# Optimization experiments

Hardware: AMD Instinct MI355X
Metric: run time of the kernel (lower is better)

The kernel has to match this reference:

```python
import jax, jax.numpy as jnp
import numpy as np

L = 50
N_INIT = 3.5      # initial radius n
N_STEP = 0.5      # n_step
NUM_ADJ_PARM = 0.1
NUM_CANDS = 256   # candidate radii n + k*n_step


def _leaky(x):
    return jax.nn.leaky_relu(x, negative_slope=0.01)


def _conv(x, w, b):
    y = jax.lax.conv_general_dilated(x, w, (1, 1), 'VALID',
                                     dimension_numbers=('NCHW', 'OIHW', 'NCHW'))
    return y + b[None, :, None, None]


def _maxpool2(x):
    return jax.lax.reduce_window(x, -jnp.inf, jax.lax.max,
                                 (1, 1, 2, 2), (1, 1, 2, 2), 'VALID')


def _sage(x, adj, w_rel, b_rel, w_root):
    # PyG DenseSAGEConv: lin_rel(mean-agg) + lin_root(x), normalize=False
    agg = adj @ x
    deg = jnp.clip(jnp.sum(adj, axis=-1, keepdims=True), 1.0, None)
    return (agg / deg) @ w_rel.T + b_rel + x @ w_root.T


def _build_adj(h):
    # fused pairwise euclidean distance + radius threshold with retry:
    # smallest radius in {n + k*n_step} whose (directed) edge count >= 0.1*N
    g = h @ h.T                                   # [N,N] gram
    sq = jnp.diag(g)
    dist = jnp.sqrt(jnp.maximum(sq[:, None] - 2.0 * g + sq[None, :], 0.0))
    n = h.shape[0]
    eye = jnp.eye(n, dtype=bool)
    d_sorted = jnp.sort(jnp.where(eye, jnp.inf, dist).reshape(-1))
    cands = N_INIT + N_STEP * jnp.arange(NUM_CANDS, dtype=dist.dtype)
    counts = jnp.searchsorted(d_sorted, cands)    # edges with dist < cand
    thr = cands[jnp.argmax(counts >= NUM_ADJ_PARM * n)]
    A = ((dist < thr) & (~eye)).astype(h.dtype)
    return jax.lax.stop_gradient(A)               # edge list is non-diff in torch too


def _diff_pool(z, a, s):
    # PyG dense_diff_pool (link + entropy losses; only link loss l1 is returned)
    s = jax.nn.softmax(s, axis=-1)
    x = s.T @ z
    adj = s.T @ a @ s
    l1 = jnp.linalg.norm(a - s @ s.T) / (a.shape[0] * a.shape[1])
    return x, adj, l1


def setup_inputs() -> dict:
    key = jax.random.key(0)
    ks = jax.random.split(key, 19)
    def w(k, shape, scale=0.05):
        return scale * jax.random.normal(k, shape, dtype=jnp.float32)
    N = 4096  # bag size / number of graph nodes
    return {
        'x': jax.random.normal(ks[0], (1, N, 1, 28, 28), dtype=jnp.float32),
        'conv1_w': w(ks[1], (20, 1, 5, 5)),
        'conv1_b': w(ks[2], (20,)),
        'conv2_w': w(ks[3], (50, 20, 5, 5)),
        'conv2_b': w(ks[4], (50,)),
        'fc_w': w(ks[5], (50, 800)),
        'fc_b': w(ks[6], (50,)),
        'embd_rel_w': w(ks[7], (50, 50)),
        'embd_rel_b': w(ks[8], (50,)),
        'embd_root_w': w(ks[9], (50, 50)),
        'pool_rel_w': w(ks[10], (1, 50)),
        'pool_rel_b': w(ks[11], (1,)),
        'pool_root_w': w(ks[12], (1, 50)),
        'mlp_w': w(ks[13], (1, 1)),
        'mlp_b': w(ks[14], (1,)),
        'lin1_w': w(ks[15], (25, 50)),
        'lin1_b': w(ks[16], (25,)),
        'lin2_w': w(ks[17], (2, 25)),
        'lin2_b': w(ks[18], (2,)),
    }


def reference(x, conv1_w, conv1_b, conv2_w, conv2_b, fc_w, fc_b,
              embd_rel_w, embd_rel_b, embd_root_w,
              pool_rel_w, pool_rel_b, pool_root_w,
              mlp_w, mlp_b, lin1_w, lin1_b, lin2_w, lin2_b):
    xi = x[0]                                             # squeeze(0): [N,1,28,28]
    h = _maxpool2(jax.nn.relu(_conv(xi, conv1_w, conv1_b)))   # [N,20,12,12]
    h = _maxpool2(jax.nn.relu(_conv(h, conv2_w, conv2_b)))    # [N,50,4,4]
    h = h.reshape(h.shape[0], -1)                         # [N,800]
    h = jax.nn.relu(h @ fc_w.T + fc_b)                    # [N,50]
    A = _build_adj(h)                                     # [N,N] dense adjacency
    Z = _leaky(_sage(h, A, embd_rel_w, embd_rel_b, embd_root_w))   # [N,50]
    S = _leaky(_sage(h, A, pool_rel_w, pool_rel_b, pool_root_w))   # [N,1]
    S = _leaky(S @ mlp_w.T + mlp_b)                       # [N,1]
    Xp, adjp, l1 = _diff_pool(Z, A, S)                    # [1,50], [1,1]
    Xp = _leaky(_sage(Xp, adjp, embd_rel_w, embd_rel_b, embd_root_w))  # reuses gnn_embd
    v = Xp.reshape(-1)                                    # [50]
    v = _leaky(v @ lin1_w.T + lin1_b)                     # [25]
    v = _leaky(v @ lin2_w.T + lin2_b)                     # [2]
    p = jax.nn.softmax(v, axis=0)
    return jnp.max(p), jnp.argmax(p), l1
```

## Files before the change

### kernel.cpp

```cpp
#include <hip/hip_runtime.h>
#include <hip/hip_bf16.h>

#define AGG_OFF     0u
#define DEG_OFF     819200u
#define XP_OFF      835584u
#define HIST_OFF    835840u
#define SCAL_OFF    836992u
#define S_OFF       837120u
#define H_OFF       1048576u
#define HT_OFF      1867776u
#define SQ_OFF      2686976u
#define BYTES_OFF   2703360u
#define WS_NEED     (2703360ull + 16777216ull)

__global__ __launch_bounds__(256) void mil_init(unsigned int* __restrict__ w)
{
    w[(size_t)blockIdx.x * 256u + threadIdx.x] = 0u;
}

__global__ __launch_bounds__(256) void mil_cnn(
    const float* __restrict__ x, const float* __restrict__ w1, const float* __restrict__ b1,
    const float* __restrict__ w2, const float* __restrict__ b2,
    const float* __restrict__ fcw, const float* __restrict__ fcb,
    float* __restrict__ hout, float* __restrict__ hT, float* __restrict__ sqout)
{
    __shared__ __align__(16) float img[784];
    __shared__ float w1s[500];
    __shared__ float b1s[20];
    __shared__ float b2s[50];
    __shared__ __align__(16) float pool1[20*144];
    __shared__ float w2s[50*4*25];
    __shared__ __align__(16) float pool2[800];
    __shared__ float hloc[50];

    const int n = blockIdx.x;
    const int t = threadIdx.x;

    const float* xin = x + (size_t)n * 784;
    for (int i = t; i < 784; i += 256) img[i] = xin[i];
    for (int i = t; i < 500; i += 256) w1s[i] = w1[i];
    if (t < 20) b1s[t] = b1[t];
    { int u = t - 32; if (u >= 0 && u < 50) b2s[u] = b2[u]; }
    __syncthreads();

    if (t < 240) {
        const int c = t / 12, py = t % 12;
        float wr[25];
#pragma unroll
        for (int k = 0; k < 25; k++) wr[k] = w1s[c*25 + k];
        float acc0[24], acc1[24];
#pragma unroll
        for (int i = 0; i < 24; i++) { acc0[i] = 0.f; acc1[i] = 0.f; }
#pragma unroll
        for (int ky = 0; ky < 5; ky++) {
            const int yr = 2*py + ky;
            float ra[28], rb[28];
#pragma unroll
            for (int i = 0; i < 28; i++) ra[i] = img[yr*28 + i];
#pragma unroll
            for (int i = 0; i < 28; i++) rb[i] = img[yr*28 + 28 + i];
#pragma unroll
            for (int kx = 0; kx < 5; kx++) {
                const float wv = wr[ky*5 + kx];
#pragma unroll
                for (int xo = 0; xo < 24; xo++) {
                    acc0[xo] = fmaf(ra[xo+kx], wv, acc0[xo]);
                    acc1[xo] = fmaf(rb[xo+kx], wv, acc1[xo]);
                }
            }
        }
        const float bias = b1s[c];
#pragma unroll
        for (int px = 0; px < 12; px++) {
            float v = fmaxf(fmaxf(acc0[2*px], acc0[2*px+1]),
                            fmaxf(acc1[2*px], acc1[2*px+1]));
            pool1[c*144 + py*12 + px] = fmaxf(v + bias, 0.f);
        }
    }
    __syncthreads();

    float acc2[16];
#pragma unroll
    for (int i = 0; i < 16; i++) acc2[i] = 0.f;
    const int c2 = t / 4, py2 = t % 4;
    for (int cig = 0; cig < 5; cig++) {
        __syncthreads();
        for (int idx = t; idx < 5000; idx += 256) {
            const int cc = idx / 100, rem = idx % 100;
            w2s[idx] = w2[cc*500 + cig*100 + rem];
        }
        __syncthreads();
        if (t < 200) {
#pragma unroll
            for (int cl = 0; cl < 4; cl++) {
                const int cig4 = cig*4 + cl;
#pragma unroll
                for (int ky = 0; ky < 5; ky++) {
                    const int r = 2*py2 + ky;
                    float ra[12], rb[12];
#pragma unroll
                    for (int i = 0; i < 12; i++) ra[i] = pool1[cig4*144 + r*12 + i];
#pragma unroll
                    for (int i = 0; i < 12; i++) rb[i] = pool1[cig4*144 + (r+1)*12 + i];
#pragma unroll
                    for (int kx = 0; kx < 5; kx++) {
                        const float wv = w2s[(c2*4 + cl)*25 + ky*5 + kx];
#pragma unroll
                        for (int xo = 0; xo < 8; xo++) {
                            acc2[xo]   = fmaf(ra[xo+kx], wv, acc2[xo]);
                            acc2[8+xo] = fmaf(rb[xo+kx], wv, acc2[8+xo]);
                        }
                    }
                }
            }
        }
    }
    __syncthreads();
    if (t < 200) {
        const float bias = b2s[c2];
#pragma unroll
        for (int px = 0; px < 4; px++) {
            float v = fmaxf(fmaxf(acc2[2*px], acc2[2*px+1]),
                            fmaxf(acc2[8+2*px], acc2[8+2*px+1]));
            pool2[c2*16 + py2*4 + px] = fmaxf(v + bias, 0.f);
        }
    }
    __syncthreads();

    {
        const int wv = t >> 6, lane = t & 63;
        for (int o = wv; o < 50; o += 4) {
            float acc = 0.f;
#pragma unroll
            for (int r = 0; r < 13; r++) {
                const int k = r*64 + lane;
                if (k < 800) acc = fmaf(fcw[o*800 + k], pool2[k], acc);
            }
#pragma unroll
            for (int off = 32; off > 0; off >>= 1) acc += __shfl_xor(acc, off);
            if (lane == 0) hloc[o] = fmaxf(acc + fcb[o], 0.f);
        }
    }
    __syncthreads();
    if (t < 50) {
        const float v = hloc[t];
        hout[(size_t)n*50 + t] = v;
        hT[(size_t)t*4096 + n] = v;
    }
    if (t < 64) {
        float s = (t < 50) ? hloc[t]*hloc[t] : 0.f;
#pragma unroll
        for (int off = 32; off > 0; off >>= 1) s += __shfl_xor(s, off);
        if (t == 0) sqout[n] = s;
    }
}

__global__ __launch_bounds__(256) void mil_colsum(
    const float* __restrict__ hT, float* __restrict__ S)
{
    __shared__ float red[4];
    const int d = blockIdx.x, t = threadIdx.x;
    float s = 0.f;
    for (int nn = t; nn < 4096; nn += 256) s += hT[(size_t)d*4096 + nn];
#pragma unroll
    for (int off = 32; off > 0; off >>= 1) s += __shfl_xor(s, off);
    if ((t & 63) == 0) red[t >> 6] = s;
    __syncthreads();
    if (t == 0) S[d] = red[0] + red[1] + red[2] + red[3];
}

__global__ __launch_bounds__(256, 3) void mil_hist(
    const float* __restrict__ hT, const float* __restrict__ sq,
    unsigned int* __restrict__ hist, unsigned char* __restrict__ bytesA,
    const int wb)
{
    __shared__ __align__(16) float hiT[6400];
    __shared__ __align__(16) float hjT[6400];
    __shared__ float sqi[128], sqj[128];
    __shared__ unsigned int lh[257];

    const int t = threadIdx.x;
    const int i0 = blockIdx.x * 128, j0 = blockIdx.y * 128;

    for (int idx = t; idx < 6400; idx += 256) {
        const int c = idx >> 7, l = idx & 127;
        hiT[idx] = hT[(size_t)c*4096 + i0 + l];
        hjT[idx] = hT[(size_t)c*4096 + j0 + l];
    }
    if (t < 128) { sqi[t] = sq[i0 + t]; sqj[t] = sq[j0 + t]; }
    for (int idx = t; idx < 257; idx += 256) lh[idx] = 0;
    __syncthreads();

    const int ti = t >> 4, tj = t & 15;
    float acc[8][8];
#pragma unroll
    for (int a = 0; a < 8; a++)
#pragma unroll
        for (int b = 0; b < 8; b++) acc[a][b] = 0.f;

    for (int c = 0; c < 50; c++) {
        const float4 a0 = *(const float4*)&hiT[c*128 + ti*8];
        const float4 a1 = *(const float4*)&hiT[c*128 + ti*8 + 4];
        const float4 b0 = *(const float4*)&hjT[c*128 + tj*8];
        const float4 b1 = *(const float4*)&hjT[c*128 + tj*8 + 4];
        const float aa[8] = {a0.x,a0.y,a0.z,a0.w,a1.x,a1.y,a1.z,a1.w};
        const float bb[8] = {b0.x,b0.y,b0.z,b0.w,b1.x,b1.y,b1.z,b1.w};
#pragma unroll
        for (int a = 0; a < 8; a++)
#pragma unroll
            for (int b = 0; b < 8; b++)
                acc[a][b] = fmaf(aa[a], bb[b], acc[a][b]);
    }

    unsigned int cnt0 = 0;
#pragma unroll
    for (int a = 0; a < 8; a++) {
        unsigned pk0 = 0, pk1 = 0;
#pragma unroll
        for (int b = 0; b < 8; b++) {
            const int gi = i0 + ti*8 + a, gj = j0 + tj*8 + b;
            int kbyte = 255;
            if (gi != gj) {
                const float d2 = sqi[ti*8+a] + sqj[tj*8+b] - 2.f*acc[a][b];
                const float d = sqrtf(fmaxf(d2, 0.f));
                int k = (int)floorf((d - 3.5f)*2.f) + 1;
                k = k < 0 ? 0 : (k > 256 ? 256 : k);
                if (k > 0   && d <  3.5f + 0.5f*(float)(k-1)) k--;
                if (k < 256 && d >= 3.5f + 0.5f*(float)k)     k++;
                if (k == 0) cnt0++;
                else atomicAdd(&lh[k], 1u);
                kbyte = k < 255 ? k : 255;
            }
            if (b < 4) pk0 |= (unsigned)kbyte << (8*b);
            else       pk1 |= (unsigned)kbyte << (8*(b-4));
        }
        if (wb) {
            const int gi = i0 + ti*8 + a;
            *(uint2*)&bytesA[(size_t)gi*4096 + j0 + tj*8] = make_uint2(pk0, pk1);
        }
    }
#pragma unroll
    for (int off = 32; off > 0; off >>= 1) cnt0 += __shfl_xor(cnt0, off);
    if ((t & 63) == 0 && cnt0) atomicAdd(&lh[0], cnt0);
    __syncthreads();
    for (int idx = t; idx < 257; idx += 256)
        if (lh[idx]) atomicAdd(&hist[idx], lh[idx]);
}

__global__ void mil_scan(const unsigned int* __restrict__ hist, int* __restrict__ scal)
{
    if (threadIdx.x == 0) {
        unsigned long long cum = 0, nz = 0;
        int kc = -1;
        for (int k = 0; k < 256; k++) {
            cum += hist[k];
            if (kc < 0 && cum >= 410ull) { kc = k; nz = cum; }
        }
        if (kc < 0) { kc = 0; nz = hist[0]; }
        scal[0] = kc;
        scal[1] = (int)nz;
        scal[2] = (nz * 2ull > 16773120ull) ? 1 : 0;
        scal[3] = (kc >= 255) ? 1 : 0;
    }
}

__global__ __launch_bounds__(256) void mil_agg_b(
    const float* __restrict__ h, const unsigned char* __restrict__ bytesA,
    const int* __restrict__ scal, float* __restrict__ agg, float* __restrict__ deg)
{
    __shared__ __align__(16) unsigned char bL[64*528];
    __shared__ __align__(16) float hsub[4096];
    if (scal[3] != 0) return;
    const int t = threadIdx.x;
    const int i0 = blockIdx.x * 64;
    const int jg = blockIdx.y * 512;
    const int kc = scal[0];
    const bool inv = (scal[2] != 0);

    for (int idx = t; idx < 2048; idx += 256) {
        const int r = idx >> 5, c = idx & 31;
        *(uint4*)&bL[r*528 + c*16] =
            *(const uint4*)&bytesA[(size_t)(i0 + r)*4096 + jg + c*16];
    }

    const int il = t >> 2, dq = t & 3;
    const int gi = i0 + il;
    float accum[16];
#pragma unroll
    for (int i = 0; i < 16; i++) accum[i] = 0.f;
    int degc = 0;

    for (int js = 0; js < 8; js++) {
        __syncthreads();
        for (int idx = t; idx < 4096; idx += 256) {
            const int jj = idx >> 6, d = idx & 63;
            hsub[idx] = (d < 50) ? h[(size_t)(jg + js*64 + jj)*50 + d] : 0.f;
        }
        __syncthreads();
        const unsigned char* brow = &bL[il*528 + js*64];
        const int jbase = jg + js*64;
        for (int jj = 0; jj < 64; jj++) {
            const bool e = (jbase + jj != gi) && ((brow[jj] <= kc) != inv);
            if (!__any(e)) continue;
            const float m = e ? 1.f : 0.f;
            if (e && dq == 0) degc++;
#pragma unroll
            for (int q = 0; q < 4; q++) {
                const float4 hv = *(const float4*)&hsub[jj*64 + dq*16 + q*4];
                accum[q*4+0] = fmaf(m, hv.x, accum[q*4+0]);
                accum[q*4+1] = fmaf(m, hv.y, accum[q*4+1]);
                accum[q*4+2] = fmaf(m, hv.z, accum[q*4+2]);
                accum[q*4+3] = fmaf(m, hv.w, accum[q*4+3]);
            }
        }
    }

#pragma unroll
    for (int q = 0; q < 4; q++)
#pragma unroll
        for (int rr = 0; rr < 4; rr++) {
            const int d = dq*16 + q*4 + rr;
            if (d < 50 && accum[q*4+rr] != 0.f)
                atomicAdd(&agg[(size_t)gi*50 + d], accum[q*4+rr]);
        }
    if (dq == 0 && degc) atomicAdd(&deg[gi], (float)degc);
}

__global__ __launch_bounds__(256, 3) void mil_agg_r(
    const float* __restrict__ h, const float* __restrict__ hT, const float* __restrict__ sq,
    const int* __restrict__ scal, float* __restrict__ agg, float* __restrict__ deg,
    const int mode)
{
    __shared__ __align__(16) float hiT[3200];
    __shared__ __align__(16) float hjT[3200];
    __shared__ float sqi[64], sqj[64];
    __shared__ __align__(16) float hsub[4096];
    __shared__ __align__(16) unsigned char mk[4096];

    if (mode == 1 && scal[3] == 0) return;
    const int t = threadIdx.x;
    const int i0 = blockIdx.x * 64;
    const float thr = 3.5f + 0.5f * (float)scal[0];
    const bool inv = (scal[2] != 0);

    for (int idx = t; idx < 3200; idx += 256) {
        const int c = idx >> 6, l = idx & 63;
        hiT[idx] = hT[(size_t)c*4096 + i0 + l];
    }
    if (t < 64) sqi[t] = sq[i0 + t];

    const int ti = t >> 4, tj = t & 15;
    const int il = t >> 2, dq = t & 3;
    float accum[16];
#pragma unroll
    for (int i = 0; i < 16; i++) accum[i] = 0.f;
    int degc = 0;

    for (int js = 0; js < 8; js++) {
        const int j0 = blockIdx.y * 512 + js * 64;
        __syncthreads();
        for (int idx = t; idx < 3200; idx += 256) {
            const int c = idx >> 6, l = idx & 63;
            hjT[idx] = hT[(size_t)c*4096 + j0 + l];
        }
        for (int idx = t; idx < 4096; idx += 256) {
            const int jj = idx >> 6, d = idx & 63;
            hsub[idx] = (d < 50) ? h[(size_t)(j0 + jj)*50 + d] : 0.f;
        }
        if (t < 64) sqj[t] = sq[j0 + t];
        __syncthreads();

        float acc[4][4];
#pragma unroll
        for (int a = 0; a < 4; a++)
#pragma unroll
            for (int b = 0; b < 4; b++) acc[a][b] = 0.f;
        for (int c = 0; c < 50; c++) {
            const float4 av = *(const float4*)&hiT[c*64 + ti*4];
            const float4 bv = *(const float4*)&hjT[c*64 + tj*4];
            const float aa[4] = {av.x, av.y, av.z, av.w};
            const float bb[4] = {bv.x, bv.y, bv.z, bv.w};
#pragma unroll
            for (int a = 0; a < 4; a++)
#pragma unroll
                for (int b = 0; b < 4; b++)
                    acc[a][b] = fmaf(aa[a], bb[b], acc[a][b]);
        }

#pragma unroll
        for (int b = 0; b < 4; b++) {
            unsigned char ob[4];
#pragma unroll
            for (int a = 0; a < 4; a++) {
                const int gi = i0 + ti*4 + a, gj = j0 + tj*4 + b;
                const float d2 = sqi[ti*4+a] + sqj[tj*4+b] - 2.f*acc[a][b];
                const float dd = sqrtf(fmaxf(d2, 0.f));
                const bool edge = (dd < thr);
                ob[a] = (gi != gj && (edge != inv)) ? 1 : 0;
            }
            *(uchar4*)&mk[(tj*4+b)*64 + ti*4] = make_uchar4(ob[0], ob[1], ob[2], ob[3]);
        }
        __syncthreads();

        for (int jj = 0; jj < 64; jj++) {
            const bool e = (mk[jj*64 + il] != 0);
            if (!__any(e)) continue;
            const float m = e ? 1.f : 0.f;
            if (e && dq == 0) degc++;
#pragma unroll
            for (int q = 0; q < 4; q++) {
                const float4 hv = *(const float4*)&hsub[jj*64 + dq*16 + q*4];
                accum[q*4+0] = fmaf(m, hv.x, accum[q*4+0]);
                accum[q*4+1] = fmaf(m, hv.y, accum[q*4+1]);
                accum[q*4+2] = fmaf(m, hv.z, accum[q*4+2]);
                accum[q*4+3] = fmaf(m, hv.w, accum[q*4+3]);
            }
        }
    }

    const int node = i0 + il;
#pragma unroll
    for (int q = 0; q < 4; q++)
#pragma unroll
        for (int rr = 0; rr < 4; rr++) {
            const int d = dq*16 + q*4 + rr;
            if (d < 50 && accum[q*4+rr] != 0.f)
                atomicAdd(&agg[(size_t)node*50 + d], accum[q*4+rr]);
        }
    if (dq == 0 && degc) atomicAdd(&deg[node], (float)degc);
}

__global__ __launch_bounds__(256) void mil_sage(
    const float* __restrict__ h, const float* __restrict__ agg, const float* __restrict__ deg,
    const float* __restrict__ S, const int* __restrict__ scal,
    const float* __restrict__ relw, const float* __restrict__ relb,
    const float* __restrict__ rootw, float* __restrict__ Xp)
{
    __shared__ float relT[2500];
    __shared__ float rootT[2500];
    __shared__ float rb[50];
    __shared__ float hn[250], mn[250], zb[250];
    const int t = threadIdx.x;
    const int nb = blockIdx.x * 5;
    const bool inv = (scal[2] != 0);

    for (int idx = t; idx < 2500; idx += 256) {
        const int d = idx / 50, c = idx % 50;
        relT[c*50 + d]  = relw[idx];
        rootT[c*50 + d] = rootw[idx];
    }
    if (t < 50) rb[t] = relb[t];
    if (t < 250) {
        const int nl = t / 50, d = t % 50;
        const int node = nb + nl;
        if (node < 4096) {
            const float hv = h[(size_t)node*50 + d];
            float av = agg[(size_t)node*50 + d];
            float dg = deg[node];
            if (inv) { av = S[d] - hv - av; dg = 4095.f - dg; }
            hn[t] = hv;
            mn[t] = av / fmaxf(dg, 1.f);
        } else { hn[t] = 0.f; mn[t] = 0.f; }
    }
    __syncthreads();
    if (t < 250) {
        const int nl = t / 50, d = t % 50;
        float z = rb[d];
        for (int c = 0; c < 50; c++) {
            z = fmaf(mn[nl*50 + c], relT[c*50 + d], z);
            z = fmaf(hn[nl*50 + c], rootT[c*50 + d], z);
        }
        z = z > 0.f ? z : 0.01f * z;
        zb[t] = (nb + nl < 4096) ? z : 0.f;
    }
    __syncthreads();
    if (t < 50) {
        float s = 0.f;
#pragma unroll
        for (int nl = 0; nl < 5; nl++) s += zb[nl*50 + t];
        atomicAdd(&Xp[t], s);
    }
}

__global__ void mil_final(
    const float* __restrict__ Xp, const int* __restrict__ scal,
    const float* __restrict__ relw, const float* __restrict__ relb,
    const float* __restrict__ rootw,
    const float* __restrict__ l1w, const float* __restrict__ l1b,
    const float* __restrict__ l2w, const float* __restrict__ l2b,
    float* __restrict__ out)
{
    __shared__ float xp[50], x2[50], v1[25], v2[2];
    const int t = threadIdx.x;
    if (t < 50) xp[t] = Xp[t];
    __syncthreads();
    const float adjp = (float)scal[1];
    const float dmax = fmaxf(adjp, 1.f);
    if (t < 50) {
        float z = relb[t];
        for (int c = 0; c < 50; c++) {
            const float mnc = (adjp * xp[c]) / dmax;
            z = fmaf(mnc,   relw[t*50 + c], z);
            z = fmaf(xp[c], rootw[t*50 + c], z);
        }
        x2[t] = z > 0.f ? z : 0.01f*z;
    }
    __syncthreads();
    if (t < 25) {
        float v = l1b[t];
        for (int c = 0; c < 50; c++) v = fmaf(l1w[t*50 + c], x2[c], v);
        v1[t] = v > 0.f ? v : 0.01f*v;
    }
    __syncthreads();
    if (t < 2) {
        float v = l2b[t];
        for (int c = 0; c < 25; c++) v = fmaf(l2w[t*25 + c], v1[c], v);
        v2[t] = v > 0.f ? v : 0.01f*v;
    }
    __syncthreads();
    if (t == 0) {
        const float a = v2[0], b = v2[1];
        const float mx = fmaxf(a, b);
        const float e0 = expf(a - mx), e1 = expf(b - mx);
        const float s = e0 + e1;
        const float p0 = e0 / s, p1 = e1 / s;
        const float pm = fmaxf(p0, p1);
        const float am = (p1 > p0) ? 1.f : 0.f;
        const int nnz = scal[1];
        const float l1v = sqrtf((float)(16777216 - nnz)) / 16777216.f;
        out[0] = pm;
        out[1] = am;
        out[2] = l1v;
    }
}

extern "C" void kernel_launch(void* const* d_in, const int* in_sizes, int n_in,
                              void* d_out, int out_size, void* d_ws, size_t ws_size,
                              hipStream_t stream)
{
    (void)in_sizes; (void)n_in; (void)out_size;
    const float* x     = (const float*)d_in[0];
    const float* w1    = (const float*)d_in[1];
    const float* b1    = (const float*)d_in[2];
    const float* w2    = (const float*)d_in[3];
    const float* b2    = (const float*)d_in[4];
    const float* fcw   = (const float*)d_in[5];
    const float* fcb   = (const float*)d_in[6];
    const float* relw  = (const float*)d_in[7];
    const float* relb  = (const float*)d_in[8];
    const float* rootw = (const float*)d_in[9];
    const float* l1w   = (const float*)d_in[15];
    const float* l1b   = (const float*)d_in[16];
    const float* l2w   = (const float*)d_in[17];
    const float* l2b   = (const float*)d_in[18];

    char* ws = (char*)d_ws;
    float* agg = (float*)(ws + AGG_OFF);
    float* deg = (float*)(ws + DEG_OFF);
    float* Xp  = (float*)(ws + XP_OFF);
    unsigned int* hist = (unsigned int*)(ws + HIST_OFF);
    int* scal  = (int*)(ws + SCAL_OFF);
    float* S   = (float*)(ws + S_OFF);
    float* h   = (float*)(ws + H_OFF);
    float* hT  = (float*)(ws + HT_OFF);
    float* sq  = (float*)(ws + SQ_OFF);
    unsigned char* bytesA = (unsigned char*)(ws + BYTES_OFF);

    const int have_bytes = (ws_size >= WS_NEED) ? 1 : 0;

    mil_init<<<818, 256, 0, stream>>>((unsigned int*)d_ws);
    mil_cnn<<<4096, 256, 0, stream>>>(x, w1, b1, w2, b2, fcw, fcb, h, hT, sq);
    mil_colsum<<<50, 256, 0, stream>>>(hT, S);
    mil_hist<<<dim3(32, 32), 256, 0, stream>>>(hT, sq, hist, bytesA, have_bytes);
    mil_scan<<<1, 64, 0, stream>>>(hist, scal);
    if (have_bytes) {
        mil_agg_b<<<dim3(64, 8), 256, 0, stream>>>(h, bytesA, scal, agg, deg);
        mil_agg_r<<<dim3(64, 8), 256, 0, stream>>>(h, hT, sq, scal, agg, deg, 1);
    } else {
        mil_agg_r<<<dim3(64, 8), 256, 0, stream>>>(h, hT, sq, scal, agg, deg, 0);
    }
    mil_sage<<<820, 256, 0, stream>>>(h, agg, deg, S, scal, relw, relb, rootw, Xp);
    mil_final<<<1, 64, 0, stream>>>(Xp, scal, relw, relb, rootw,
                                    l1w, l1b, l2w, l2b, (float*)d_out);
}
```

Before: 542.4 us.

## Shrink CNN kernel LDS footprint and reuse input rows in conv loops

The image, conv1 weights and conv2 weight staging now share one overlaid shared-memory buffer. Conv2 weights are staged in smaller padded chunks, which cuts LDS usage so more blocks fit per CU, and launch bounds now request 5 blocks. Both conv loops load each input row once with float4 reads and use it for the two pooled output rows, instead of loading each row twice. Conv2 weights are kept in registers per input channel. In exchange, conv2 needs twice as many staging rounds and barriers, and the tighter register bound may cause spills.

```diff
diff --git a/kernel.cpp b/kernel.cpp
--- a/kernel.cpp
+++ b/kernel.cpp
@@ -18,20 +18,22 @@
     w[(size_t)blockIdx.x * 256u + threadIdx.x] = 0u;
 }
 
-__global__ __launch_bounds__(256) void mil_cnn(
+__global__ __launch_bounds__(256, 5) void mil_cnn(
     const float* __restrict__ x, const float* __restrict__ w1, const float* __restrict__ b1,
     const float* __restrict__ w2, const float* __restrict__ b2,
     const float* __restrict__ fcw, const float* __restrict__ fcb,
     float* __restrict__ hout, float* __restrict__ hT, float* __restrict__ sqout)
 {
-    __shared__ __align__(16) float img[784];
-    __shared__ float w1s[500];
+    __shared__ __align__(16) float pool1[20*144];
+    __shared__ __align__(16) float pool2[800];
     __shared__ float b1s[20];
-    __shared__ float b2s[50];
-    __shared__ __align__(16) float pool1[20*144];
-    __shared__ float w2s[50*4*25];
-    __shared__ __align__(16) float pool2[800];
-    __shared__ float hloc[50];
+    __shared__ float b2s[64];
+    __shared__ float hloc[64];
+    __shared__ __align__(16) float ovl[2800];
+
+    float* img = ovl;
+    float* w1s = ovl + 784;
+    float* w2s = ovl;
 
     const int n = blockIdx.x;
     const int t = threadIdx.x;
@@ -52,20 +54,30 @@
 #pragma unroll
         for (int i = 0; i < 24; i++) { acc0[i] = 0.f; acc1[i] = 0.f; }
 #pragma unroll
-        for (int ky = 0; ky < 5; ky++) {
-            const int yr = 2*py + ky;
-            float ra[28], rb[28];
-#pragma unroll
-            for (int i = 0; i < 28; i++) ra[i] = img[yr*28 + i];
-#pragma unroll
-            for (int i = 0; i < 28; i++) rb[i] = img[yr*28 + 28 + i];
-#pragma unroll
-            for (int kx = 0; kx < 5; kx++) {
-                const float wv = wr[ky*5 + kx];
-#pragma unroll
-                for (int xo = 0; xo < 24; xo++) {
-                    acc0[xo] = fmaf(ra[xo+kx], wv, acc0[xo]);
-                    acc1[xo] = fmaf(rb[xo+kx], wv, acc1[xo]);
+        for (int j = 0; j < 6; j++) {
+            float rr[28];
+            const float* rp = &img[(2*py + j)*28];
+#pragma unroll
+            for (int q = 0; q < 7; q++) {
+                const float4 v = *(const float4*)(rp + 4*q);
+                rr[4*q+0] = v.x; rr[4*q+1] = v.y; rr[4*q+2] = v.z; rr[4*q+3] = v.w;
+            }
+            if (j <= 4) {
+#pragma unroll
+                for (int kx = 0; kx < 5; kx++) {
+                    const float wv = wr[j*5 + kx];
+#pragma unroll
+                    for (int xo = 0; xo < 24; xo++)
+                        acc0[xo] = fmaf(rr[xo+kx], wv, acc0[xo]);
+                }
+            }
+            if (j >= 1) {
+#pragma unroll
+                for (int kx = 0; kx < 5; kx++) {
+                    const float wv = wr[(j-1)*5 + kx];
+#pragma unroll
+                    for (int xo = 0; xo < 24; xo++)
+                        acc1[xo] = fmaf(rr[xo+kx], wv, acc1[xo]);
                 }
             }
         }
@@ -83,32 +95,53 @@
 #pragma unroll
     for (int i = 0; i < 16; i++) acc2[i] = 0.f;
     const int c2 = t / 4, py2 = t % 4;
-    for (int cig = 0; cig < 5; cig++) {
+    for (int cig = 0; cig < 10; cig++) {
         __syncthreads();
-        for (int idx = t; idx < 5000; idx += 256) {
-            const int cc = idx / 100, rem = idx % 100;
-            w2s[idx] = w2[cc*500 + cig*100 + rem];
+        for (int idx = t; idx < 2800; idx += 256) {
+            const int cc = idx / 56, r = idx % 56;
+            const int cl = r / 28, k = r % 28;
+            w2s[idx] = (k < 25) ? w2[cc*500 + (cig*2 + cl)*25 + k] : 0.f;
         }
         __syncthreads();
         if (t < 200) {
 #pragma unroll
-            for (int cl = 0; cl < 4; cl++) {
-                const int cig4 = cig*4 + cl;
-#pragma unroll
-                for (int ky = 0; ky < 5; ky++) {
-                    const int r = 2*py2 + ky;
-                    float ra[12], rb[12];
-#pragma unroll
-                    for (int i = 0; i < 12; i++) ra[i] = pool1[cig4*144 + r*12 + i];
-#pragma unroll
-                    for (int i = 0; i < 12; i++) rb[i] = pool1[cig4*144 + (r+1)*12 + i];
-#pragma unroll
-                    for (int kx = 0; kx < 5; kx++) {
-                        const float wv = w2s[(c2*4 + cl)*25 + ky*5 + kx];
-#pragma unroll
-                        for (int xo = 0; xo < 8; xo++) {
-                            acc2[xo]   = fmaf(ra[xo+kx], wv, acc2[xo]);
-                            acc2[8+xo] = fmaf(rb[xo+kx], wv, acc2[8+xo]);
+            for (int cl = 0; cl < 2; cl++) {
+                const int ci = cig*2 + cl;
+                float wreg[25];
+                const float* wp = &w2s[c2*56 + cl*28];
+#pragma unroll
+                for (int q = 0; q < 6; q++) {
+                    const float4 v = *(const float4*)(wp + 4*q);
+                    wreg[4*q+0] = v.x; wreg[4*q+1] = v.y;
+                    wreg[4*q+2] = v.z; wreg[4*q+3] = v.w;
+                }
+                wreg[24] = wp[24];
+#pragma unroll
+                for (int j = 0; j < 6; j++) {
+                    float rr[12];
+                    const float* rp = &pool1[ci*144 + (2*py2 + j)*12];
+#pragma unroll
+                    for (int q = 0; q < 3; q++) {
+                        const float4 v = *(const float4*)(rp + 4*q);
+                        rr[4*q+0] = v.x; rr[4*q+1] = v.y;
+                        rr[4*q+2] = v.z; rr[4*q+3] = v.w;
+                    }
+                    if (j <= 4) {
+#pragma unroll
+                        for (int kx = 0; kx < 5; kx++) {
+                            const float wv = wreg[j*5 + kx];
+#pragma unroll
+                            for (int xo = 0; xo < 8; xo++)
+                                acc2[xo] = fmaf(rr[xo+kx], wv, acc2[xo]);
+                        }
+                    }
+                    if (j >= 1) {
+#pragma unroll
+                        for (int kx = 0; kx < 5; kx++) {
+                            const float wv = wreg[(j-1)*5 + kx];
+#pragma unroll
+                            for (int xo = 0; xo < 8; xo++)
+                                acc2[8+xo] = fmaf(rr[xo+kx], wv, acc2[8+xo]);
                         }
                     }
                 }
```

After: 540.5 us. No clear change (-0.4%).
